# Kernel optimization log

Hardware: AMD Instinct MI355X
Metric: run time of the kernel (lower is better)

The kernel has to match this reference:

```python
import jax, jax.numpy as jnp
import numpy as np
import math

D_MODEL = 512
KEY_DIM = 128
NUM_LAYERS = 2
TEMP = 30.0
NORM_EPS = 1e-5
NORM_SCALE = math.sqrt(1.0 / (D_MODEL * 4 * 4))


def _l2norm_lastdim(x):
    # F.normalize(x, p=2, dim=-1): x / max(||x||, 1e-12)
    n = jnp.sqrt(jnp.sum(x * x, axis=-1, keepdims=True))
    return x / jnp.maximum(n, 1e-12)


def _attn(q, k, v, WK, bK):
    # q: [Sq,B,D], k: [Sk,B,D], v: [Sk,B,D] -> [Sq,B,D]
    wq = _l2norm_lastdim(q @ WK + bK)            # [Sq,B,K]
    wk = _l2norm_lastdim(k @ WK + bK)            # [Sk,B,K]
    dot = jnp.einsum('qbk,sbk->bqs', wq, wk)     # cosine sims
    aff = jax.nn.softmax(dot * TEMP, axis=-1)
    return jnp.einsum('bqs,sbd->qbd', aff, v)


def _instance_norm(x, h, w):
    # x: [HW,B,D]; InstanceL2Norm over (D,h,w) per batch element, size_average=True
    HW, B, D = x.shape
    ss = jnp.sum(x * x, axis=(0, 2))             # [B]
    factor = NORM_SCALE * jnp.sqrt((D * h * w) / (ss + NORM_EPS))
    return x * factor[None, :, None]


def _encoder(src4d, WKs, bKs):
    B, D, H, W = src4d.shape
    x = src4d.reshape(B, D, H * W).transpose(2, 0, 1)   # [HW,B,D]
    for _ in range(NUM_LAYERS):
        x = _instance_norm(x + _attn(x, x, x, WKs, bKs), H, W)
    return x  # memory [HW,B,D]


def _decoder(tgt4d, memory, pos, WKs, bKs, WKc, bKc):
    B, D, H, W = tgt4d.shape
    x = tgt4d.reshape(B, D, H * W).transpose(2, 0, 1)   # [HW,B,D]
    for _ in range(NUM_LAYERS):
        x = _instance_norm(x + _attn(x, x, x, WKs, bKs), H, W)
        mask = _attn(x, memory, pos, WKc, bKc)
        t2 = _instance_norm(x * mask, H, W)
        t3 = _attn(x, memory, memory * pos, WKc, bKc)
        t4 = _instance_norm(x + t3, H, W)
        x = _instance_norm(t2 + t4, H, W)
    feat = x.reshape(H, W, B, D).transpose(2, 3, 0, 1)  # [B,D,H,W]
    return feat


def setup_inputs() -> dict:
    key = jax.random.key(0)
    k1, k2, k3, k4, k5 = jax.random.split(key, 5)
    B, D, H, W = 16, D_MODEL, 32, 32
    std = math.sqrt(2.0 / KEY_DIM)
    return {
        'train_feat': jax.random.normal(k1, (B, D, H, W), jnp.float32),
        'test_feat': jax.random.normal(k2, (B, D, H, W), jnp.float32),
        'train_label': jax.random.uniform(k3, (B, H, W), jnp.float32),
        'WK_self': jax.random.normal(k4, (D, KEY_DIM), jnp.float32) * std,
        'bK_self': jnp.zeros((KEY_DIM,), jnp.float32),
        'WK_cross': jax.random.normal(k5, (D, KEY_DIM), jnp.float32) * std,
        'bK_cross': jnp.zeros((KEY_DIM,), jnp.float32),
    }


def reference(train_feat, test_feat, train_label, WK_self, bK_self, WK_cross, bK_cross):
    B, D, H, W = train_feat.shape
    memory = _encoder(train_feat, WK_self, bK_self)              # [HW,B,D]
    # pos: label [B,H,W] -> [HW,B,1] -> broadcast to [HW,B,D]
    pos = jnp.broadcast_to(train_label.reshape(B, H * W).T[:, :, None], (H * W, B, D))
    encoded_feat = _decoder(train_feat, memory, pos, WK_self, bK_self, WK_cross, bK_cross)
    decoded_feat = _decoder(test_feat, memory, pos, WK_self, bK_self, WK_cross, bK_cross)
    return (encoded_feat, decoded_feat)
```

## Files before the change

### kernel.cpp

```cpp
#include <hip/hip_runtime.h>
#include <math.h>

#define NB 16
#define SEQ 1024
#define DM 512
#define KD 128
#define TEMP_F 30.0f
#define NS_F 0.011048543456039805f
#define DS_F 524288.0f

#define SS_IDX(grp, b) (((grp) * NB + (b)) * 16)
#define SS_STRIDE 768
#define SS_STAGES 12
#define SS_FLOATS (SS_STRIDE * SS_STAGES)

typedef short bf16x8 __attribute__((ext_vector_type(8)));
typedef float f32x4 __attribute__((ext_vector_type(4)));
typedef unsigned short us;
typedef unsigned short us4v __attribute__((ext_vector_type(4)));
typedef unsigned short us8 __attribute__((ext_vector_type(8)));

__device__ __forceinline__ us f2bf(float x) {
    union { float f; unsigned u; } v; v.f = x;
    unsigned r = v.u + 0x7fffu + ((v.u >> 16) & 1u);
    return (us)(r >> 16);
}
__device__ __forceinline__ float bf2f(us h) {
    union { unsigned u; float f; } v; v.u = ((unsigned)h) << 16;
    return v.f;
}

#define GLL16(gp, lp) __builtin_amdgcn_global_load_lds( \
    (__attribute__((address_space(1))) void*)(unsigned long long)(gp), \
    (__attribute__((address_space(3))) void*)(unsigned)(unsigned long long)(lp), 16, 0, 0)

__global__ __launch_bounds__(256) void k_transpose_in(const float* __restrict__ src,
                                                      us* __restrict__ XC,
                                                      us* __restrict__ XT) {
    __shared__ float tile[32][33];
    const int b = blockIdx.z;
    const int d0 = blockIdx.x * 32;
    const int s0 = blockIdx.y * 32;
    const int tx = threadIdx.x, ty = threadIdx.y;
    const float* p = src + (size_t)b * DM * SEQ;
    us* pt = XT + (size_t)b * DM * SEQ;
    us* pc = XC + (size_t)b * SEQ * 1024;
#pragma unroll
    for (int j = 0; j < 32; j += 8) {
        const size_t o = (size_t)(d0 + ty + j) * SEQ + s0 + tx;
        const float v = p[o];
        tile[ty + j][tx] = v;
        pt[o] = f2bf(v);
    }
    __syncthreads();
#pragma unroll
    for (int j = 0; j < 4; ++j) {
        const int s = s0 + ty + j * 8;
        const int d = d0 + tx;
        const float v = tile[tx][ty + j * 8];
        const us h = f2bf(v);
        pc[(size_t)s * 1024 + d] = h;
        pc[(size_t)s * 1024 + 512 + d] = f2bf(v - bf2f(h));
    }
}

__global__ __launch_bounds__(256) void k_mklabel(const us* __restrict__ MT,
                                                 const float* __restrict__ label,
                                                 us* __restrict__ ML) {
    const int b = blockIdx.y;
    const size_t off = ((size_t)blockIdx.x * 256 + threadIdx.x) * 8;
    const int s = (int)(off & (SEQ - 1));
    const size_t o = (size_t)b * DM * SEQ + off;
    us8 v = *(const us8*)(MT + o);
    const float4 l0 = *(const float4*)(label + (size_t)b * SEQ + s);
    const float4 l1 = *(const float4*)(label + (size_t)b * SEQ + s + 4);
    us8 r;
    r[0] = f2bf(bf2f(v[0]) * l0.x); r[1] = f2bf(bf2f(v[1]) * l0.y);
    r[2] = f2bf(bf2f(v[2]) * l0.z); r[3] = f2bf(bf2f(v[3]) * l0.w);
    r[4] = f2bf(bf2f(v[4]) * l1.x); r[5] = f2bf(bf2f(v[5]) * l1.y);
    r[6] = f2bf(bf2f(v[6]) * l1.z); r[7] = f2bf(bf2f(v[7]) * l1.w);
    *(us8*)(ML + o) = r;
}

__global__ __launch_bounds__(256) void k_wsplit(const float* __restrict__ WK,
                                                us* __restrict__ WC) {
    const int k = blockIdx.x;
    for (int d = threadIdx.x; d < DM; d += 256) {
        const float v = WK[(size_t)d * KD + k];
        const us h = f2bf(v);
        WC[(size_t)k * 1024 + d] = h;
        WC[(size_t)k * 1024 + 512 + d] = f2bf(v - bf2f(h));
    }
}

__global__ __launch_bounds__(256) void k_proj(const us* __restrict__ XC,
                                              const us* __restrict__ WC,
                                              const float* __restrict__ bK,
                                              us* __restrict__ Wout) {
    const int row0 = blockIdx.x * 32;
    __shared__ short As[32 * 64], Bs[128 * 64];
    __shared__ float ssp[2][32];
    const int tid = threadIdx.x, w = tid >> 6, l = tid & 63;
    const int wm = (w >> 1) * 16, wn = (w & 1) * 64;
    const int sr = l >> 3, sc = (((l & 7) ^ (l >> 3)) << 3);
    const int lr = l & 15, lk = (l >> 4) * 8;
    const int sx = (lr & 7) << 3;
    f32x4 acc[4] = {};
    for (int k0 = 0; k0 < 1536; k0 += 64) {
        const int ak0 = (k0 < 1024) ? k0 : k0 - 1024;
        const int bk0 = (k0 < 512) ? k0 : k0 - 512;
        GLL16(XC + (size_t)(row0 + w * 8 + sr) * 1024 + ak0 + sc, &As[w * 512]);
#pragma unroll
        for (int cc = 0; cc < 4; ++cc) {
            const int c = 4 * w + cc;
            GLL16(WC + (size_t)(c * 8 + sr) * 1024 + bk0 + sc, &Bs[c * 512]);
        }
        __syncthreads();
#pragma unroll
        for (int kc = 0; kc < 2; ++kc) {
            const int kk = kc * 32 + lk;
            const bf16x8 a = *(const bf16x8*)&As[(wm + lr) * 64 + (kk ^ sx)];
            bf16x8 bb[4];
#pragma unroll
            for (int fn = 0; fn < 4; ++fn)
                bb[fn] = *(const bf16x8*)&Bs[(wn + fn * 16 + lr) * 64 + (kk ^ sx)];
#pragma unroll
            for (int fn = 0; fn < 4; ++fn)
                acc[fn] = __builtin_amdgcn_mfma_f32_16x16x32_bf16(a, bb[fn], acc[fn], 0, 0, 0);
        }
        __syncthreads();
    }
    const int er = l & 15, eq = (l >> 4) * 4;
    const int nh = w & 1;
    float bkv[4];
#pragma unroll
    for (int fn = 0; fn < 4; ++fn) bkv[fn] = bK[wn + fn * 16 + er];
    float vv[4][4];
#pragma unroll
    for (int r = 0; r < 4; ++r) {
        float ss = 0.f;
#pragma unroll
        for (int fn = 0; fn < 4; ++fn) {
            const float t = acc[fn][r] + bkv[fn];
            vv[fn][r] = t;
            ss += t * t;
        }
#pragma unroll
        for (int o = 8; o > 0; o >>= 1) ss += __shfl_xor(ss, o, 64);
        if (er == 0) ssp[nh][wm + eq + r] = ss;
    }
    __syncthreads();
#pragma unroll
    for (int r = 0; r < 4; ++r) {
        const int rowloc = wm + eq + r;
        const float tot = ssp[0][rowloc] + ssp[1][rowloc];
        const float invn = 1.0f / fmaxf(sqrtf(tot), 1e-12f);
        const size_t ro = (size_t)(row0 + rowloc) * 256;
#pragma unroll
        for (int fn = 0; fn < 4; ++fn) {
            const float ov = vv[fn][r] * invn;
            const us h = f2bf(ov);
            Wout[ro + wn + fn * 16 + er] = h;
            Wout[ro + 128 + wn + fn * 16 + er] = f2bf(ov - bf2f(h));
        }
    }
}

__global__ __launch_bounds__(512, 2) void k_attn(const us* __restrict__ Qc,
                                                 const us* __restrict__ Kc,
                                                 const us* __restrict__ VT,
                                                 const us* __restrict__ XC,
                                                 const float* __restrict__ labelp,
                                                 float* __restrict__ MVEC,
                                                 float* __restrict__ Cout,
                                                 float* __restrict__ SS, int mode) {
    const int b = blockIdx.x;
    const int q0 = blockIdx.y * 64;
    __shared__ short KL[2][4 * 32 * 64];
    __shared__ us PL[64 * 40];
    __shared__ float RSL[2][64], RLL[2][64];
    __shared__ float INVL[64], MVL[64];
    __shared__ float LBL[1024];
    __shared__ float ps[3][8];
    const int tid = threadIdx.x, w = tid >> 6, l = tid & 63;
    const int lr = l & 15, g = l >> 4, lk = g * 8;
    const int qa = w & 3, sh = w >> 2;
    const int kx = (lr & 7) << 3;
    const us* Qb = Qc + (size_t)b * SEQ * 256;
    const us* Kb = Kc + (size_t)b * SEQ * 256;
    const us* Vb = VT + (size_t)b * DM * SEQ;

    const us* Qrow = Qb + (size_t)(q0 + qa * 16 + lr) * 256;
    bf16x8 qh[4], ql[4];
#pragma unroll
    for (int kc = 0; kc < 4; ++kc) {
        qh[kc] = *(const bf16x8*)(Qrow + kc * 32 + lk);
        ql[kc] = *(const bf16x8*)(Qrow + 128 + kc * 32 + lk);
    }
#pragma unroll
    for (int i = 0; i < 2; ++i) {
        const int c = w * 2 + i, p = c >> 2, rg = c & 3;
        GLL16(Kb + (size_t)(rg * 8 + (l >> 3)) * 256 + p * 64 + (((l & 7) ^ (l >> 3)) << 3),
              &KL[0][p * 2048 + rg * 512 + l * 8]);
    }
    if (mode == 2 && w < 4)
        GLL16(labelp + (size_t)b * SEQ + w * 256 + l * 4, &LBL[w * 256 + l * 4]);
    __syncthreads();

    f32x4 acc[4][4];
#pragma unroll
    for (int m = 0; m < 4; ++m)
#pragma unroll
        for (int n = 0; n < 4; ++n) acc[m][n] = (f32x4){0.f, 0.f, 0.f, 0.f};
    float rs = 0.f, rl = 0.f;
    int cur = 0;
    for (int it = 0; it < 32; ++it) {
        const int s0 = it * 32;
        bf16x8 vb[4];
#pragma unroll
        for (int n = 0; n < 4; ++n)
            vb[n] = *(const bf16x8*)(Vb + (size_t)(w * 64 + n * 16 + lr) * 1024 + s0 + lk);
        const int rowb = (sh * 16 + lr) * 64;
        f32x4 sacc = {};
        bf16x8 kf[4];
#pragma unroll
        for (int kc = 0; kc < 4; ++kc)
            kf[kc] = *(const bf16x8*)&KL[cur][(kc >> 1) * 2048 + rowb + ((((kc & 1) << 5) + lk) ^ kx)];
        __builtin_amdgcn_s_setprio(1);
#pragma unroll
        for (int kc = 0; kc < 4; ++kc)
            sacc = __builtin_amdgcn_mfma_f32_16x16x32_bf16(kf[kc], qh[kc], sacc, 0, 0, 0);
#pragma unroll
        for (int kc = 0; kc < 4; ++kc)
            sacc = __builtin_amdgcn_mfma_f32_16x16x32_bf16(kf[kc], ql[kc], sacc, 0, 0, 0);
        __builtin_amdgcn_s_setprio(0);
#pragma unroll
        for (int kc = 0; kc < 4; ++kc)
            kf[kc] = *(const bf16x8*)&KL[cur][(2 + (kc >> 1)) * 2048 + rowb + ((((kc & 1) << 5) + lk) ^ kx)];
        __builtin_amdgcn_s_setprio(1);
#pragma unroll
        for (int kc = 0; kc < 4; ++kc)
            sacc = __builtin_amdgcn_mfma_f32_16x16x32_bf16(kf[kc], qh[kc], sacc, 0, 0, 0);
        __builtin_amdgcn_s_setprio(0);
        const int sbase = sh * 16 + g * 4;
        float lb4[4] = {0.f, 0.f, 0.f, 0.f};
        if (mode == 2) {
            const float4 t = *(const float4*)&LBL[s0 + sbase];
            lb4[0] = t.x; lb4[1] = t.y; lb4[2] = t.z; lb4[3] = t.w;
        }
        us4v pw;
#pragma unroll
        for (int r = 0; r < 4; ++r) {
            const float e = __expf(fmaf(TEMP_F, sacc[r], -TEMP_F));
            rs += e;
            rl += e * lb4[r];
            pw[r] = f2bf(e);
        }
        *(us4v*)&PL[(qa * 16 + lr) * 40 + sbase] = pw;
        __syncthreads();
        if (it < 31) {
            const int s1 = s0 + 32, nb2 = cur ^ 1;
#pragma unroll
            for (int i = 0; i < 2; ++i) {
                const int c = w * 2 + i, p = c >> 2, rg = c & 3;
                GLL16(Kb + (size_t)(s1 + rg * 8 + (l >> 3)) * 256 + p * 64 + (((l & 7) ^ (l >> 3)) << 3),
                      &KL[nb2][p * 2048 + rg * 512 + l * 8]);
            }
        }
        bf16x8 pa[4];
#pragma unroll
        for (int m = 0; m < 4; ++m)
            pa[m] = *(const bf16x8*)&PL[(m * 16 + lr) * 40 + lk];
        __builtin_amdgcn_s_setprio(1);
#pragma unroll
        for (int m = 0; m < 4; ++m)
#pragma unroll
            for (int n = 0; n < 4; ++n)
                acc[m][n] = __builtin_amdgcn_mfma_f32_16x16x32_bf16(pa[m], vb[n], acc[m][n], 0, 0, 0);
        __builtin_amdgcn_s_setprio(0);
        __syncthreads();
        cur ^= 1;
    }

    rs += __shfl_xor(rs, 16, 64);
    rs += __shfl_xor(rs, 32, 64);
    rl += __shfl_xor(rl, 16, 64);
    rl += __shfl_xor(rl, 32, 64);
    if (g == 0) {
        RSL[sh][qa * 16 + lr] = rs;
        RLL[sh][qa * 16 + lr] = rl;
    }
    __syncthreads();
    if (tid < 64) {
        const float tot = RSL[0][tid] + RSL[1][tid];
        const float iv = 1.0f / tot;
        INVL[tid] = iv;
        const float mvv = (RLL[0][tid] + RLL[1][tid]) * iv;
        MVL[tid] = mvv;
        if (mode == 2) MVEC[(size_t)b * SEQ + q0 + tid] = mvv;
    }
    __syncthreads();

    const us* XCb = XC + (size_t)b * SEQ * 1024;
    float sa = 0.f, sb = 0.f, sab = 0.f;
#pragma unroll
    for (int m = 0; m < 4; ++m)
#pragma unroll
        for (int r = 0; r < 4; ++r) {
            const int q = m * 16 + g * 4 + r;
            const float iv = INVL[q];
            const float mvq = MVL[q];
            const int row = q0 + q;
#pragma unroll
            for (int n = 0; n < 4; ++n) {
                const int col = w * 64 + n * 16 + lr;
                float v = acc[m][n][r] * iv;
                const size_t o = ((size_t)b * SEQ + row) * DM + col;
                const size_t xo = (size_t)row * 1024 + col;
                const float x = bf2f(XCb[xo]) + bf2f(XCb[xo + 512]);
                v += x;
                sb += v * v;
                if (mode == 2) { const float a = x * mvq; sa += a * a; sab += a * v; }
                Cout[o] = v;
            }
        }
#pragma unroll
    for (int off = 32; off > 0; off >>= 1) {
        sb += __shfl_xor(sb, off, 64);
        if (mode == 2) { sa += __shfl_xor(sa, off, 64); sab += __shfl_xor(sab, off, 64); }
    }
    if (l == 0) { ps[0][w] = sb; ps[1][w] = sa; ps[2][w] = sab; }
    __syncthreads();
    if (tid == 0) {
        float t0 = 0.f, t1 = 0.f, t2 = 0.f;
#pragma unroll
        for (int i = 0; i < 8; ++i) { t0 += ps[0][i]; t1 += ps[1][i]; t2 += ps[2][i]; }
        if (mode == 1) {
            atomicAdd(&SS[SS_IDX(0, b)], t0);
        } else {
            atomicAdd(&SS[SS_IDX(0, b)], t1);
            atomicAdd(&SS[SS_IDX(1, b)], t0);
            atomicAdd(&SS[SS_IDX(2, b)], t2);
        }
    }
}

__global__ void k_zero(float* __restrict__ SSb) {
    const int i = blockIdx.x * 256 + threadIdx.x;
    if (i < SS_FLOATS) SSb[i] = 0.0f;
}

__global__ __launch_bounds__(256) void k_finish(const float* __restrict__ Tin,
                                                const us* __restrict__ XCin,
                                                const float* __restrict__ mv,
                                                const float* __restrict__ SS,
                                                us* __restrict__ XCout,
                                                us* __restrict__ XTb,
                                                float* __restrict__ XTf,
                                                int mode, int writeXC) {
    const int b = blockIdx.z;
    const int s0 = blockIdx.x * 32, d0 = blockIdx.y * 32;
    const int tx = threadIdx.x, ty = threadIdx.y;
    __shared__ float tile[32][33];
    float f1 = 0.f, f2 = 0.f, f3;
    if (mode == 0) {
        f3 = NS_F * sqrtf(DS_F / (SS[SS_IDX(0, b)] + 1e-5f));
    } else {
        const float ssa = SS[SS_IDX(0, b)], ssb = SS[SS_IDX(1, b)], ssab = SS[SS_IDX(2, b)];
        f1 = NS_F * sqrtf(DS_F / (ssa + 1e-5f));
        f2 = NS_F * sqrtf(DS_F / (ssb + 1e-5f));
        const float ssc = f1 * f1 * ssa + 2.f * f1 * f2 * ssab + f2 * f2 * ssb;
        f3 = NS_F * sqrtf(DS_F / (ssc + 1e-5f));
    }
#pragma unroll
    for (int j = 0; j < 4; ++j) {
        const int s = s0 + ty + j * 8;
        const int d = d0 + tx;
        const size_t o = ((size_t)b * SEQ + s) * DM + d;
        const size_t xo = ((size_t)b * SEQ + s) * 1024 + d;
        float v;
        if (mode == 0) v = f3 * Tin[o];
        else {
            const float x = bf2f(XCin[xo]) + bf2f(XCin[xo + 512]);
            v = f3 * (f1 * x * mv[(size_t)b * SEQ + s] + f2 * Tin[o]);
        }
        if (writeXC) {
            const us h = f2bf(v);
            XCout[xo] = h;
            XCout[xo + 512] = f2bf(v - bf2f(h));
        }
        tile[ty + j * 8][tx] = v;
    }
    __syncthreads();
#pragma unroll
    for (int j = 0; j < 4; ++j) {
        const int d = d0 + ty + j * 8;
        const int s = s0 + tx;
        const float v = tile[tx][ty + j * 8];
        const size_t o = ((size_t)b * DM + d) * SEQ + s;
        if (XTb) XTb[o] = f2bf(v);
        else if (XTf) XTf[o] = v;
    }
}

extern "C" void kernel_launch(void* const* d_in, const int* in_sizes, int n_in,
                              void* d_out, int out_size, void* d_ws, size_t ws_size,
                              hipStream_t stream) {
    const float* train_feat = (const float*)d_in[0];
    const float* test_feat  = (const float*)d_in[1];
    const float* label      = (const float*)d_in[2];
    const float* WKs        = (const float*)d_in[3];
    const float* bKs        = (const float*)d_in[4];
    const float* WKc        = (const float*)d_in[5];
    const float* bKc        = (const float*)d_in[6];
    float* out = (float*)d_out;
    float* w = (float*)d_ws;

    const size_t SBD = (size_t)NB * SEQ * DM;
    const size_t SBK = (size_t)NB * SEQ * KD;

    float* T   = w;
    us* XC     = (us*)(T + SBD);
    us* XTd    = XC + 2 * SBD;
    us* MEMT   = XTd + SBD;
    us* MEMLT  = MEMT + SBD;
    us* W1C    = MEMLT + SBD;
    us* WKMC   = W1C + 2 * SBK;
    us* WCs    = WKMC + 2 * SBK;
    us* WCc    = WCs + (size_t)KD * 1024;
    float* MVEC = (float*)(WCc + (size_t)KD * 1024);
    float* SS   = MVEC + (size_t)NB * SEQ;

    const dim3 gT_in(DM / 32, SEQ / 32, NB), bT(32, 8);
    const dim3 gFin(SEQ / 32, DM / 32, NB);
    const dim3 gAtt(NB, SEQ / 64);

    int stage = 0;
    auto nextSS = [&]() { return SS + (size_t)(stage++) * SS_STRIDE; };

    k_zero<<<(SS_FLOATS + 255) / 256, 256, 0, stream>>>(SS);
    k_wsplit<<<KD, 256, 0, stream>>>(WKs, WCs);
    k_wsplit<<<KD, 256, 0, stream>>>(WKc, WCc);

    k_transpose_in<<<gT_in, bT, 0, stream>>>(train_feat, XC, MEMT);
    for (int l = 0; l < 2; ++l) {
        float* SSst = nextSS();
        k_proj<<<NB * SEQ / 32, 256, 0, stream>>>(XC, WCs, bKs, W1C);
        k_attn<<<gAtt, 512, 0, stream>>>(W1C, W1C, MEMT, XC, nullptr, nullptr, T, SSst, 1);
        k_finish<<<gFin, bT, 0, stream>>>(T, XC, nullptr, SSst, XC, MEMT, nullptr, 0, 1);
    }
    k_proj<<<NB * SEQ / 32, 256, 0, stream>>>(XC, WCc, bKc, WKMC);
    k_mklabel<<<dim3(DM * SEQ / 8 / 256, NB), 256, 0, stream>>>(MEMT, label, MEMLT);

    auto decoder = [&](const float* feat, float* outp) {
        k_transpose_in<<<gT_in, bT, 0, stream>>>(feat, XC, XTd);
        for (int l = 0; l < 2; ++l) {
            float* SSst = nextSS();
            k_proj<<<NB * SEQ / 32, 256, 0, stream>>>(XC, WCs, bKs, W1C);
            k_attn<<<gAtt, 512, 0, stream>>>(W1C, W1C, XTd, XC, nullptr, nullptr, T, SSst, 1);
            k_finish<<<gFin, bT, 0, stream>>>(T, XC, nullptr, SSst, XC, XTd, nullptr, 0, 1);
            float* SSst2 = nextSS();
            k_proj<<<NB * SEQ / 32, 256, 0, stream>>>(XC, WCc, bKc, W1C);
            k_attn<<<gAtt, 512, 0, stream>>>(W1C, WKMC, MEMLT, XC, label, MVEC, T, SSst2, 2);
            if (l == 0)
                k_finish<<<gFin, bT, 0, stream>>>(T, XC, MVEC, SSst2, XC, XTd, nullptr, 1, 1);
            else
                k_finish<<<gFin, bT, 0, stream>>>(T, XC, MVEC, SSst2, XC, nullptr, outp, 1, 0);
        }
    };
    decoder(train_feat, out);
    decoder(test_feat, out + SBD);
}
```

Before: 1.028 ms.

## Double key tile to 64 per iteration and read labels from global

The attention kernel now handles 64 keys per loop iteration instead of 32. This halves the number of block-wide barriers and K-tile refills, and each wave computes two 16-key score subtiles before the P·V product. The label staging in shared memory is removed, so labels are read straight from global memory as float4. The cost is more LDS for K and P and more live registers (two sets of V fragments), which could hurt occupancy at launch bounds of 2 blocks per CU.

```diff
diff --git a/kernel.cpp b/kernel.cpp
--- a/kernel.cpp
+++ b/kernel.cpp
@@ -13,6 +13,8 @@
 #define SS_STRIDE 768
 #define SS_STAGES 12
 #define SS_FLOATS (SS_STRIDE * SS_STAGES)
+
+#define PSTR 72
 
 typedef short bf16x8 __attribute__((ext_vector_type(8)));
 typedef float f32x4 __attribute__((ext_vector_type(4)));
@@ -176,11 +178,10 @@
                                                  float* __restrict__ SS, int mode) {
     const int b = blockIdx.x;
     const int q0 = blockIdx.y * 64;
-    __shared__ short KL[2][4 * 32 * 64];
-    __shared__ us PL[64 * 40];
+    __shared__ short KL[2][4 * 64 * 64];
+    __shared__ us PL[64 * PSTR];
     __shared__ float RSL[2][64], RLL[2][64];
     __shared__ float INVL[64], MVL[64];
-    __shared__ float LBL[1024];
     __shared__ float ps[3][8];
     const int tid = threadIdx.x, w = tid >> 6, l = tid & 63;
     const int lr = l & 15, g = l >> 4, lk = g * 8;
@@ -189,6 +190,7 @@
     const us* Qb = Qc + (size_t)b * SEQ * 256;
     const us* Kb = Kc + (size_t)b * SEQ * 256;
     const us* Vb = VT + (size_t)b * DM * SEQ;
+    const float* Lb = labelp ? labelp + (size_t)b * SEQ : nullptr;
 
     const us* Qrow = Qb + (size_t)(q0 + qa * 16 + lr) * 256;
     bf16x8 qh[4], ql[4];
@@ -198,13 +200,11 @@
         ql[kc] = *(const bf16x8*)(Qrow + 128 + kc * 32 + lk);
     }
 #pragma unroll
-    for (int i = 0; i < 2; ++i) {
-        const int c = w * 2 + i, p = c >> 2, rg = c & 3;
+    for (int i = 0; i < 4; ++i) {
+        const int c = w * 4 + i, p = c & 3, rg = c >> 2;
         GLL16(Kb + (size_t)(rg * 8 + (l >> 3)) * 256 + p * 64 + (((l & 7) ^ (l >> 3)) << 3),
-              &KL[0][p * 2048 + rg * 512 + l * 8]);
-    }
-    if (mode == 2 && w < 4)
-        GLL16(labelp + (size_t)b * SEQ + w * 256 + l * 4, &LBL[w * 256 + l * 4]);
+              &KL[0][p * 4096 + rg * 512 + l * 8]);
+    }
     __syncthreads();
 
     f32x4 acc[4][4];
@@ -214,69 +214,87 @@
         for (int n = 0; n < 4; ++n) acc[m][n] = (f32x4){0.f, 0.f, 0.f, 0.f};
     float rs = 0.f, rl = 0.f;
     int cur = 0;
-    for (int it = 0; it < 32; ++it) {
-        const int s0 = it * 32;
-        bf16x8 vb[4];
+    for (int it = 0; it < 16; ++it) {
+        const int s0 = it * 64;
+        bf16x8 vb0[4];
 #pragma unroll
         for (int n = 0; n < 4; ++n)
-            vb[n] = *(const bf16x8*)(Vb + (size_t)(w * 64 + n * 16 + lr) * 1024 + s0 + lk);
-        const int rowb = (sh * 16 + lr) * 64;
-        f32x4 sacc = {};
-        bf16x8 kf[4];
-#pragma unroll
-        for (int kc = 0; kc < 4; ++kc)
-            kf[kc] = *(const bf16x8*)&KL[cur][(kc >> 1) * 2048 + rowb + ((((kc & 1) << 5) + lk) ^ kx)];
+            vb0[n] = *(const bf16x8*)(Vb + (size_t)(w * 64 + n * 16 + lr) * 1024 + s0 + lk);
+#pragma unroll
+        for (int sn = 0; sn < 2; ++sn) {
+            const int srow = sh * 32 + sn * 16 + lr;
+            const int rowb = srow * 64;
+            f32x4 sacc = {};
+            bf16x8 kf[4];
+#pragma unroll
+            for (int kc = 0; kc < 4; ++kc)
+                kf[kc] = *(const bf16x8*)&KL[cur][(kc >> 1) * 4096 + rowb + ((((kc & 1) << 5) + lk) ^ kx)];
+            __builtin_amdgcn_s_setprio(1);
+#pragma unroll
+            for (int kc = 0; kc < 4; ++kc)
+                sacc = __builtin_amdgcn_mfma_f32_16x16x32_bf16(kf[kc], qh[kc], sacc, 0, 0, 0);
+#pragma unroll
+            for (int kc = 0; kc < 4; ++kc)
+                sacc = __builtin_amdgcn_mfma_f32_16x16x32_bf16(kf[kc], ql[kc], sacc, 0, 0, 0);
+            __builtin_amdgcn_s_setprio(0);
+#pragma unroll
+            for (int kc = 0; kc < 4; ++kc)
+                kf[kc] = *(const bf16x8*)&KL[cur][(2 + (kc >> 1)) * 4096 + rowb + ((((kc & 1) << 5) + lk) ^ kx)];
+            __builtin_amdgcn_s_setprio(1);
+#pragma unroll
+            for (int kc = 0; kc < 4; ++kc)
+                sacc = __builtin_amdgcn_mfma_f32_16x16x32_bf16(kf[kc], qh[kc], sacc, 0, 0, 0);
+            __builtin_amdgcn_s_setprio(0);
+            const int sbase = sh * 32 + sn * 16 + g * 4;
+            float lb4[4] = {0.f, 0.f, 0.f, 0.f};
+            if (mode == 2) {
+                const float4 t = *(const float4*)(Lb + s0 + sbase);
+                lb4[0] = t.x; lb4[1] = t.y; lb4[2] = t.z; lb4[3] = t.w;
+            }
+            us4v pw;
+#pragma unroll
+            for (int r = 0; r < 4; ++r) {
+                const float e = __expf(fmaf(TEMP_F, sacc[r], -TEMP_F));
+                rs += e;
+                rl += e * lb4[r];
+                pw[r] = f2bf(e);
+            }
+            *(us4v*)&PL[(qa * 16 + lr) * PSTR + sbase] = pw;
+        }
+        __syncthreads();
+        bf16x8 vb1[4];
+#pragma unroll
+        for (int n = 0; n < 4; ++n)
+            vb1[n] = *(const bf16x8*)(Vb + (size_t)(w * 64 + n * 16 + lr) * 1024 + s0 + 32 + lk);
+        if (it < 15) {
+            const int s1 = s0 + 64, nb2 = cur ^ 1;
+#pragma unroll
+            for (int i = 0; i < 4; ++i) {
+                const int c = w * 4 + i, p = c & 3, rg = c >> 2;
+                GLL16(Kb + (size_t)(s1 + rg * 8 + (l >> 3)) * 256 + p * 64 + (((l & 7) ^ (l >> 3)) << 3),
+                      &KL[nb2][p * 4096 + rg * 512 + l * 8]);
+            }
+        }
+        bf16x8 pa[4];
+#pragma unroll
+        for (int m = 0; m < 4; ++m)
+            pa[m] = *(const bf16x8*)&PL[(m * 16 + lr) * PSTR + lk];
         __builtin_amdgcn_s_setprio(1);
 #pragma unroll
-        for (int kc = 0; kc < 4; ++kc)
-            sacc = __builtin_amdgcn_mfma_f32_16x16x32_bf16(kf[kc], qh[kc], sacc, 0, 0, 0);
-#pragma unroll
-        for (int kc = 0; kc < 4; ++kc)
-            sacc = __builtin_amdgcn_mfma_f32_16x16x32_bf16(kf[kc], ql[kc], sacc, 0, 0, 0);
+        for (int m = 0; m < 4; ++m)
+#pragma unroll
+            for (int n = 0; n < 4; ++n)
+                acc[m][n] = __builtin_amdgcn_mfma_f32_16x16x32_bf16(pa[m], vb0[n], acc[m][n], 0, 0, 0);
         __builtin_amdgcn_s_setprio(0);
 #pragma unroll
-        for (int kc = 0; kc < 4; ++kc)
-            kf[kc] = *(const bf16x8*)&KL[cur][(2 + (kc >> 1)) * 2048 + rowb + ((((kc & 1) << 5) + lk) ^ kx)];
+        for (int m = 0; m < 4; ++m)
+            pa[m] = *(const bf16x8*)&PL[(m * 16 + lr) * PSTR + 32 + lk];
         __builtin_amdgcn_s_setprio(1);
 #pragma unroll
-        for (int kc = 0; kc < 4; ++kc)
-            sacc = __builtin_amdgcn_mfma_f32_16x16x32_bf16(kf[kc], qh[kc], sacc, 0, 0, 0);
-        __builtin_amdgcn_s_setprio(0);
-        const int sbase = sh * 16 + g * 4;
-        float lb4[4] = {0.f, 0.f, 0.f, 0.f};
-        if (mode == 2) {
-            const float4 t = *(const float4*)&LBL[s0 + sbase];
-            lb4[0] = t.x; lb4[1] = t.y; lb4[2] = t.z; lb4[3] = t.w;
-        }
-        us4v pw;
-#pragma unroll
-        for (int r = 0; r < 4; ++r) {
-            const float e = __expf(fmaf(TEMP_F, sacc[r], -TEMP_F));
-            rs += e;
-            rl += e * lb4[r];
-            pw[r] = f2bf(e);
-        }
-        *(us4v*)&PL[(qa * 16 + lr) * 40 + sbase] = pw;
-        __syncthreads();
-        if (it < 31) {
-            const int s1 = s0 + 32, nb2 = cur ^ 1;
-#pragma unroll
-            for (int i = 0; i < 2; ++i) {
-                const int c = w * 2 + i, p = c >> 2, rg = c & 3;
-                GLL16(Kb + (size_t)(s1 + rg * 8 + (l >> 3)) * 256 + p * 64 + (((l & 7) ^ (l >> 3)) << 3),
-                      &KL[nb2][p * 2048 + rg * 512 + l * 8]);
-            }
-        }
-        bf16x8 pa[4];
-#pragma unroll
         for (int m = 0; m < 4; ++m)
-            pa[m] = *(const bf16x8*)&PL[(m * 16 + lr) * 40 + lk];
-        __builtin_amdgcn_s_setprio(1);
-#pragma unroll
-        for (int m = 0; m < 4; ++m)
 #pragma unroll
             for (int n = 0; n < 4; ++n)
-                acc[m][n] = __builtin_amdgcn_mfma_f32_16x16x32_bf16(pa[m], vb[n], acc[m][n], 0, 0, 0);
+                acc[m][n] = __builtin_amdgcn_mfma_f32_16x16x32_bf16(pa[m], vb1[n], acc[m][n], 0, 0, 0);
         __builtin_amdgcn_s_setprio(0);
         __syncthreads();
         cur ^= 1;
```

Result: faster. 1.007 ms (-2.1%).
